# Kernel optimization log

Hardware: AMD Instinct MI355X
Metric: run time of the kernel (lower is better)

The kernel has to match this reference:

```python
import jax, jax.numpy as jnp
import numpy as np


def setup_inputs() -> dict:
    key = jax.random.key(0)
    k1, k2 = jax.random.split(key)
    b, n, d = 8, 4096, 128
    qk = jax.random.normal(k1, (b, n, d), dtype=jnp.float32)
    v = jax.random.normal(k2, (b, n, d), dtype=jnp.float32)
    return {"qk": qk, "v": v}


def reference(qk, v):
    # qk: [b, n, d] shared query/key tensor; v: [b, n, d]
    b, n, d = qk.shape
    # keys = L2-normalized qk (F.normalize eps=1e-12); queries = raw qk
    k = qk / jnp.maximum(jnp.linalg.norm(qk, axis=-1, keepdims=True), 1e-12)
    scores = jnp.einsum('bie,bje->bij', qk, k) * (d ** -0.5)  # [b, n, n]
    # mask self-attention on the diagonal with -inf
    eye = jnp.eye(n, dtype=bool)
    scores = jnp.where(eye[None, :, :], -jnp.inf, scores)
    attn = jax.nn.softmax(scores, axis=-1)
    out = jnp.einsum('bij,bje->bie', attn, v)  # [b, n, d]
    return out
```

## Files before the change

### kernel.cpp

```cpp
#include <hip/hip_runtime.h>
#include <hip/hip_bf16.h>
#include <stdint.h>

#define BATCH 8
#define SEQN  4096
#define DIM   128
#define NT    32

typedef __attribute__((ext_vector_type(16))) float f32x16;
typedef __bf16 bf16x8 __attribute__((ext_vector_type(8)));

#define GAS __attribute__((address_space(1)))
#define LAS __attribute__((address_space(3)))

__device__ __forceinline__ ushort f2b(float x) {
  union { float f; uint32_t u; } a; a.f = x;
  uint32_t r = a.u + 0x7fffu + ((a.u >> 16) & 1u);
  return (ushort)(r >> 16);
}
__device__ __forceinline__ uint32_t pkbf(float a, float b) {
  union { __bf16 h[2]; uint32_t u; } x;
  x.h[0] = (__bf16)a; x.h[1] = (__bf16)b;
  return x.u;
}


__global__ __launch_bounds__(256) void prep_qk(
    const float* __restrict__ qk, ushort* __restrict__ qfb, ushort* __restrict__ kfb) {
  __shared__ ushort qt_l[32 * 136];
  __shared__ ushort kt_l[32 * 136];
  const int g = blockIdx.x;
  const int t = threadIdx.x;
  const int r = t >> 3, s = t & 7;
  const float* src = qk + (size_t)g * 4096 + r * 128 + s * 16;
  float x[16];
  #pragma unroll
  for (int i = 0; i < 4; ++i) {
    float4 f = ((const float4*)src)[i];
    x[4*i] = f.x; x[4*i+1] = f.y; x[4*i+2] = f.z; x[4*i+3] = f.w;
  }
  float ss = 0.f;
  #pragma unroll
  for (int i = 0; i < 16; ++i) ss += x[i] * x[i];
  ss += __shfl_xor(ss, 1, 64);
  ss += __shfl_xor(ss, 2, 64);
  ss += __shfl_xor(ss, 4, 64);
  float rn = 1.0f / fmaxf(sqrtf(ss), 1e-12f);
  const float SC = 1.44269504088896340736f / 11.313708498984761f;
  float rs = rn * SC;
  #pragma unroll
  for (int j = 0; j < 16; ++j) {
    qt_l[r * 136 + s * 16 + j] = f2b(x[j]);
    kt_l[r * 136 + s * 16 + j] = f2b(x[j] * rs);
  }
  __syncthreads();
  #pragma unroll
  for (int p = 0; p < 2; ++p) {
    int sl = t + 256 * p;
    int qli = sl & 31, grp = sl >> 5;
    union { ushort u[8]; int4 v; } tq, tk;
    #pragma unroll
    for (int j = 0; j < 8; ++j) {
      tq.u[j] = qt_l[qli * 136 + grp * 8 + j];
      tk.u[j] = kt_l[qli * 136 + grp * 8 + j];
    }
    *(int4*)(qfb + (size_t)g * 4096 + sl * 8) = tq.v;
    *(int4*)(kfb + (size_t)g * 4096 + sl * 8) = tk.v;
  }
}

__global__ __launch_bounds__(256) void prep_v(
    const float* __restrict__ v, ushort* __restrict__ vfb) {
  __shared__ ushort vt_l[32 * 136];
  const int g = blockIdx.x;
  const int t = threadIdx.x;
  const int r = t >> 3, s = t & 7;
  const float* src = v + (size_t)g * 4096 + r * 128 + s * 16;
  #pragma unroll
  for (int i = 0; i < 4; ++i) {
    float4 f = ((const float4*)src)[i];
    vt_l[r * 136 + s * 16 + 4*i]     = f2b(f.x);
    vt_l[r * 136 + s * 16 + 4*i + 1] = f2b(f.y);
    vt_l[r * 136 + s * 16 + 4*i + 2] = f2b(f.z);
    vt_l[r * 136 + s * 16 + 4*i + 3] = f2b(f.w);
  }
  __syncthreads();
  #pragma unroll
  for (int p = 0; p < 2; ++p) {
    int sl = t + 256 * p;
    int qli = sl & 31, grp = sl >> 5;
    int db = grp >> 2, ks = (grp >> 1) & 1, hh = grp & 1;
    union { ushort u[8]; int4 v; } tv;
    #pragma unroll
    for (int j = 0; j < 8; ++j)
      tv.u[j] = vt_l[(16 * ks + 8 * hh + j) * 136 + 32 * db + qli];
    *(int4*)(vfb + (size_t)g * 4096 + sl * 8) = tv.v;
  }
}

__global__ __launch_bounds__(256, 2) void attn_kernel(
    const ushort* __restrict__ qfb, const ushort* __restrict__ kfb,
    const ushort* __restrict__ vfb, float* __restrict__ out) {
  __shared__ ushort lds[40960];

  const int tid = threadIdx.x;
  const int w  = tid >> 6;
  const int l  = tid & 63;
  const int ql = l & 31;
  const int hi = l >> 5;

  const int bidx  = blockIdx.x;
  const int batch = bidx & 7;
  const int qt    = bidx >> 3;
  const int q0    = qt * 64;
  const size_t cb = (size_t)batch * 128;

  const ushort* kq = kfb + (cb + w * 32) * 4096;
  const ushort* vq = vfb + (cb + w * 32) * 4096;
  ushort* myv = lds + w * 8192;
  ushort* ldsq = lds + 32768;

  {
    const ushort* qsrc = qfb + (cb + qt * 2) * 4096 + tid * 8;
    #pragma unroll
    for (int i = 0; i < 4; ++i)
      __builtin_amdgcn_global_load_lds((const GAS uint32_t*)(qsrc + i * 2048),
          (LAS uint32_t*)(ldsq + i * 2048 + tid * 8), 16, 0, 0);
  }

#define STAGE(bsel, t_) do {                                                   \
    const ushort* vsrc_ = vq + (size_t)(t_) * 4096 + l * 8;                    \
    ushort* vdst_ = myv + (bsel) * 4096 + l * 8;                               \
    _Pragma("unroll")                                                          \
    for (int i_ = 0; i_ < 8; ++i_)                                             \
      __builtin_amdgcn_global_load_lds((const GAS uint32_t*)(vsrc_ + i_ * 512),\
          (LAS uint32_t*)(vdst_ + i_ * 512), 16, 0, 0);                        \
  } while (0)

  STAGE(0, 0);
  bf16x8 kf[8];
  {
    const ushort* kt_p = kq + l * 8;
    #pragma unroll
    for (int kc = 0; kc < 8; ++kc) kf[kc] = *(const bf16x8*)(kt_p + kc * 512);
  }
  __syncthreads();

  f32x16 o[8];
  #pragma unroll
  for (int i = 0; i < 8; ++i)
    #pragma unroll
    for (int r = 0; r < 16; ++r) o[i][r] = 0.f;
  float lsum0 = 0.f, lsum1 = 0.f;

  int buf = 0;
  for (int t = 0; t < NT; ++t) {
    if (t + 1 < NT) STAGE(buf ^ 1, t + 1);

    bf16x8 pa[2][2];
    {
      f32x16 st;
      #pragma unroll
      for (int r = 0; r < 16; ++r) st[r] = 0.f;
      const ushort* qlp = ldsq + l * 8;
      __builtin_amdgcn_s_setprio(1);
      #pragma unroll
      for (int kc = 0; kc < 8; ++kc) {
        bf16x8 qf = *(const bf16x8*)(qlp + kc * 512);
        st = __builtin_amdgcn_mfma_f32_32x32x16_bf16(kf[kc], qf, st, 0, 0, 0);
      }
      __builtin_amdgcn_s_setprio(0);
      if (w * 1024 + t * 32 == q0) {
        #pragma unroll
        for (int r = 0; r < 16; ++r) {
          int crow = (r & 3) + 8 * (r >> 2) + 4 * hi;
          if (crow == ql) st[r] = -1e30f;
        }
      }
      float p[16]; float rs_ = 0.f;
      #pragma unroll
      for (int r = 0; r < 16; ++r) { p[r] = exp2f(st[r]); rs_ += p[r]; }
      lsum0 += rs_;
      uint32_t ww[4][2];
      #pragma unroll
      for (int g4 = 0; g4 < 4; ++g4) {
        ww[g4][0] = pkbf(p[4 * g4 + 0], p[4 * g4 + 1]);
        ww[g4][1] = pkbf(p[4 * g4 + 2], p[4 * g4 + 3]);
      }
      #pragma unroll
      for (int ks = 0; ks < 2; ++ks) {
        uint32_t a0 = ww[2 * ks][0], b0 = ww[2 * ks + 1][0];
        uint32_t a1 = ww[2 * ks][1], b1 = ww[2 * ks + 1][1];
        asm volatile("v_permlane32_swap_b32 %0, %1" : "+v"(a0), "+v"(b0));
        asm volatile("v_permlane32_swap_b32 %0, %1" : "+v"(a1), "+v"(b1));
        union { uint32_t u[4]; bf16x8 v; } pb;
        pb.u[0] = a0; pb.u[1] = a1; pb.u[2] = b0; pb.u[3] = b1;
        pa[0][ks] = pb.v;
      }
    }
    {
      f32x16 st;
      #pragma unroll
      for (int r = 0; r < 16; ++r) st[r] = 0.f;
      const ushort* qlp = ldsq + 4096 + l * 8;
      __builtin_amdgcn_s_setprio(1);
      #pragma unroll
      for (int kc = 0; kc < 8; ++kc) {
        bf16x8 qf = *(const bf16x8*)(qlp + kc * 512);
        st = __builtin_amdgcn_mfma_f32_32x32x16_bf16(kf[kc], qf, st, 0, 0, 0);
      }
      __builtin_amdgcn_s_setprio(0);
      if (t + 1 < NT) {
        const ushort* kt_p = kq + (size_t)(t + 1) * 4096 + l * 8;
        #pragma unroll
        for (int kc = 0; kc < 8; ++kc) kf[kc] = *(const bf16x8*)(kt_p + kc * 512);
      }
      if (w * 1024 + t * 32 == q0 + 32) {
        #pragma unroll
        for (int r = 0; r < 16; ++r) {
          int crow = (r & 3) + 8 * (r >> 2) + 4 * hi;
          if (crow == ql) st[r] = -1e30f;
        }
      }
      float p[16]; float rs_ = 0.f;
      #pragma unroll
      for (int r = 0; r < 16; ++r) { p[r] = exp2f(st[r]); rs_ += p[r]; }
      lsum1 += rs_;
      uint32_t ww[4][2];
      #pragma unroll
      for (int g4 = 0; g4 < 4; ++g4) {
        ww[g4][0] = pkbf(p[4 * g4 + 0], p[4 * g4 + 1]);
        ww[g4][1] = pkbf(p[4 * g4 + 2], p[4 * g4 + 3]);
      }
      #pragma unroll
      for (int ks = 0; ks < 2; ++ks) {
        uint32_t a0 = ww[2 * ks][0], b0 = ww[2 * ks + 1][0];
        uint32_t a1 = ww[2 * ks][1], b1 = ww[2 * ks + 1][1];
        asm volatile("v_permlane32_swap_b32 %0, %1" : "+v"(a0), "+v"(b0));
        asm volatile("v_permlane32_swap_b32 %0, %1" : "+v"(a1), "+v"(b1));
        union { uint32_t u[4]; bf16x8 v; } pb;
        pb.u[0] = a0; pb.u[1] = a1; pb.u[2] = b0; pb.u[3] = b1;
        pa[1][ks] = pb.v;
      }
    }

    asm volatile("s_waitcnt vmcnt(16)" ::: "memory");
    __builtin_amdgcn_sched_barrier(0);

    const ushort* vlp = myv + buf * 4096 + l * 8;
    __builtin_amdgcn_s_setprio(1);
    #pragma unroll
    for (int db = 0; db < 4; ++db)
      #pragma unroll
      for (int ks = 0; ks < 2; ++ks) {
        bf16x8 vv = *(const bf16x8*)(vlp + (db * 4 + ks * 2) * 256);
        o[db]     = __builtin_amdgcn_mfma_f32_32x32x16_bf16(vv, pa[0][ks], o[db],     0, 0, 0);
        o[4 + db] = __builtin_amdgcn_mfma_f32_32x32x16_bf16(vv, pa[1][ks], o[4 + db], 0, 0, 0);
      }
    __builtin_amdgcn_s_setprio(0);
    buf ^= 1;
  }
#undef STAGE

  __syncthreads();
  float* A  = (float*)lds;
  float* Bb = A + 8448;
  float* lt = A + 16896;
  float* Lf = A + 17408;

  lt[((w * 2 + hi) * 2 + 0) * 32 + ql] = lsum0;
  lt[((w * 2 + hi) * 2 + 1) * 32 + ql] = lsum1;
  __syncthreads();
  float L0 = 0.f, L1 = 0.f;
  #pragma unroll
  for (int i = 0; i < 8; ++i) {
    L0 += lt[(i * 2 + 0) * 32 + ql];
    L1 += lt[(i * 2 + 1) * 32 + ql];
  }
  if (w == 0 && hi == 0) { Lf[ql] = 1.0f / L0; Lf[32 + ql] = 1.0f / L1; }

  if (w == 3 || w == 1) {
    float* D = (w == 3) ? A : Bb;
    #pragma unroll
    for (int c = 0; c < 2; ++c)
      #pragma unroll
      for (int db = 0; db < 4; ++db)
        #pragma unroll
        for (int g4 = 0; g4 < 4; ++g4)
          *(float4*)(D + (32 * c + ql) * 132 + 32 * db + 8 * g4 + 4 * hi) =
              make_float4(o[c * 4 + db][4 * g4], o[c * 4 + db][4 * g4 + 1],
                          o[c * 4 + db][4 * g4 + 2], o[c * 4 + db][4 * g4 + 3]);
  }
  __syncthreads();
  if (w == 2 || w == 0) {
    float* D = (w == 2) ? A : Bb;
    #pragma unroll
    for (int c = 0; c < 2; ++c)
      #pragma unroll
      for (int db = 0; db < 4; ++db)
        #pragma unroll
        for (int g4 = 0; g4 < 4; ++g4) {
          float* ptr = D + (32 * c + ql) * 132 + 32 * db + 8 * g4 + 4 * hi;
          float4 tv = *(float4*)ptr;
          tv.x += o[c * 4 + db][4 * g4];
          tv.y += o[c * 4 + db][4 * g4 + 1];
          tv.z += o[c * 4 + db][4 * g4 + 2];
          tv.w += o[c * 4 + db][4 * g4 + 3];
          *(float4*)ptr = tv;
        }
  }
  __syncthreads();
  if (w == 0 || w == 2) {
    const int ch = w >> 1;
    float* outb = out + ((size_t)batch * SEQN + q0) * DIM;
    #pragma unroll
    for (int s2 = 0; s2 < 32; ++s2) {
      const int q = 32 * ch + s2;
      const float iv = Lf[q];
      float2 a2 = *(const float2*)(A + q * 132 + 2 * l);
      float2 b2 = *(const float2*)(Bb + q * 132 + 2 * l);
      *(float2*)(outb + (size_t)q * DIM + 2 * l) =
          make_float2((a2.x + b2.x) * iv, (a2.y + b2.y) * iv);
    }
  }
}

extern "C" void kernel_launch(void* const* d_in, const int* in_sizes, int n_in,
                              void* d_out, int out_size, void* d_ws, size_t ws_size,
                              hipStream_t stream) {
  (void)in_sizes; (void)n_in; (void)out_size; (void)ws_size;
  const float* qk = (const float*)d_in[0];
  const float* v  = (const float*)d_in[1];
  float* out = (float*)d_out;
  size_t nelem = (size_t)BATCH * SEQN * DIM;
  ushort* qfb = (ushort*)d_ws;
  ushort* kfb = qfb + nelem;
  ushort* vfb = kfb + nelem;
  prep_qk<<<BATCH * SEQN / 32, 256, 0, stream>>>(qk, qfb, kfb);
  prep_v <<<BATCH * SEQN / 32, 256, 0, stream>>>(v, vfb);
  attn_kernel<<<BATCH * (SEQN / 64), 256, 0, stream>>>(qfb, kfb, vfb, out);
}
```

Measured before the change: 115.1 us.

## Fuse prep kernels and interleave the two QK MFMA chains with the K prefetch

Merges the separate qk and v preprocessing kernels into a single launch. In the attention loop, the two 32-row score tiles are now computed with interleaved MFMA chains, and the next-tile K fragment loads are issued inside that loop instead of after it. Also switches to the raw exp2 intrinsic and uses a tree reduction for the row sums. The aim is to cut launch overhead, expose more independent MFMA work, and hide K load latency, at the cost of higher register pressure from two live accumulators plus the in-flight K loads.

Measured after the change: 99.04 us. -13.9%, faster.

```diff
diff --git a/kernel.cpp b/kernel.cpp
--- a/kernel.cpp
+++ b/kernel.cpp
@@ -25,75 +25,66 @@
 }
 
 
-__global__ __launch_bounds__(256) void prep_qk(
-    const float* __restrict__ qk, ushort* __restrict__ qfb, ushort* __restrict__ kfb) {
+__global__ __launch_bounds__(256) void prep_fused(
+    const float* __restrict__ qk, const float* __restrict__ v,
+    ushort* __restrict__ qfb, ushort* __restrict__ kfb, ushort* __restrict__ vfb) {
   __shared__ ushort qt_l[32 * 136];
   __shared__ ushort kt_l[32 * 136];
+  __shared__ ushort vt_l[32 * 136];
   const int g = blockIdx.x;
   const int t = threadIdx.x;
   const int r = t >> 3, s = t & 7;
-  const float* src = qk + (size_t)g * 4096 + r * 128 + s * 16;
-  float x[16];
-  #pragma unroll
-  for (int i = 0; i < 4; ++i) {
-    float4 f = ((const float4*)src)[i];
-    x[4*i] = f.x; x[4*i+1] = f.y; x[4*i+2] = f.z; x[4*i+3] = f.w;
-  }
-  float ss = 0.f;
-  #pragma unroll
-  for (int i = 0; i < 16; ++i) ss += x[i] * x[i];
-  ss += __shfl_xor(ss, 1, 64);
-  ss += __shfl_xor(ss, 2, 64);
-  ss += __shfl_xor(ss, 4, 64);
-  float rn = 1.0f / fmaxf(sqrtf(ss), 1e-12f);
-  const float SC = 1.44269504088896340736f / 11.313708498984761f;
-  float rs = rn * SC;
-  #pragma unroll
-  for (int j = 0; j < 16; ++j) {
-    qt_l[r * 136 + s * 16 + j] = f2b(x[j]);
-    kt_l[r * 136 + s * 16 + j] = f2b(x[j] * rs);
+  {
+    const float* src = qk + (size_t)g * 4096 + r * 128 + s * 16;
+    float x[16];
+    #pragma unroll
+    for (int i = 0; i < 4; ++i) {
+      float4 f = ((const float4*)src)[i];
+      x[4*i] = f.x; x[4*i+1] = f.y; x[4*i+2] = f.z; x[4*i+3] = f.w;
+    }
+    float ss = 0.f;
+    #pragma unroll
+    for (int i = 0; i < 16; ++i) ss += x[i] * x[i];
+    ss += __shfl_xor(ss, 1, 64);
+    ss += __shfl_xor(ss, 2, 64);
+    ss += __shfl_xor(ss, 4, 64);
+    float rn = 1.0f / fmaxf(sqrtf(ss), 1e-12f);
+    const float SC = 1.44269504088896340736f / 11.313708498984761f;
+    float rs = rn * SC;
+    #pragma unroll
+    for (int j = 0; j < 16; ++j) {
+      qt_l[r * 136 + s * 16 + j] = f2b(x[j]);
+      kt_l[r * 136 + s * 16 + j] = f2b(x[j] * rs);
+    }
+  }
+  {
+    const float* src = v + (size_t)g * 4096 + r * 128 + s * 16;
+    #pragma unroll
+    for (int i = 0; i < 4; ++i) {
+      float4 f = ((const float4*)src)[i];
+      vt_l[r * 136 + s * 16 + 4*i]     = f2b(f.x);
+      vt_l[r * 136 + s * 16 + 4*i + 1] = f2b(f.y);
+      vt_l[r * 136 + s * 16 + 4*i + 2] = f2b(f.z);
+      vt_l[r * 136 + s * 16 + 4*i + 3] = f2b(f.w);
+    }
   }
   __syncthreads();
   #pragma unroll
   for (int p = 0; p < 2; ++p) {
     int sl = t + 256 * p;
     int qli = sl & 31, grp = sl >> 5;
-    union { ushort u[8]; int4 v; } tq, tk;
+    union { ushort u[8]; int4 v; } tq, tk, tv;
     #pragma unroll
     for (int j = 0; j < 8; ++j) {
       tq.u[j] = qt_l[qli * 136 + grp * 8 + j];
       tk.u[j] = kt_l[qli * 136 + grp * 8 + j];
     }
+    int db = grp >> 2, ks = (grp >> 1) & 1, hh = grp & 1;
+    #pragma unroll
+    for (int j = 0; j < 8; ++j)
+      tv.u[j] = vt_l[(16 * ks + 8 * hh + j) * 136 + 32 * db + qli];
     *(int4*)(qfb + (size_t)g * 4096 + sl * 8) = tq.v;
     *(int4*)(kfb + (size_t)g * 4096 + sl * 8) = tk.v;
-  }
-}
-
-__global__ __launch_bounds__(256) void prep_v(
-    const float* __restrict__ v, ushort* __restrict__ vfb) {
-  __shared__ ushort vt_l[32 * 136];
-  const int g = blockIdx.x;
-  const int t = threadIdx.x;
-  const int r = t >> 3, s = t & 7;
-  const float* src = v + (size_t)g * 4096 + r * 128 + s * 16;
-  #pragma unroll
-  for (int i = 0; i < 4; ++i) {
-    float4 f = ((const float4*)src)[i];
-    vt_l[r * 136 + s * 16 + 4*i]     = f2b(f.x);
-    vt_l[r * 136 + s * 16 + 4*i + 1] = f2b(f.y);
-    vt_l[r * 136 + s * 16 + 4*i + 2] = f2b(f.z);
-    vt_l[r * 136 + s * 16 + 4*i + 3] = f2b(f.w);
-  }
-  __syncthreads();
-  #pragma unroll
-  for (int p = 0; p < 2; ++p) {
-    int sl = t + 256 * p;
-    int qli = sl & 31, grp = sl >> 5;
-    int db = grp >> 2, ks = (grp >> 1) & 1, hh = grp & 1;
-    union { ushort u[8]; int4 v; } tv;
-    #pragma unroll
-    for (int j = 0; j < 8; ++j)
-      tv.u[j] = vt_l[(16 * ks + 8 * hh + j) * 136 + 32 * db + qli];
     *(int4*)(vfb + (size_t)g * 4096 + sl * 8) = tv.v;
   }
 }
@@ -151,97 +142,89 @@
   for (int i = 0; i < 8; ++i)
     #pragma unroll
     for (int r = 0; r < 16; ++r) o[i][r] = 0.f;
-  float lsum0 = 0.f, lsum1 = 0.f;
+  float ls0 = 0.f, ls1 = 0.f;
 
   int buf = 0;
   for (int t = 0; t < NT; ++t) {
     if (t + 1 < NT) STAGE(buf ^ 1, t + 1);
-
-    bf16x8 pa[2][2];
+    const bool pfK = (t + 1 < NT);
+    const ushort* kp_n = kq + (size_t)(t + 1) * 4096 + l * 8;
+
+    f32x16 st0, st1;
+    #pragma unroll
+    for (int r = 0; r < 16; ++r) { st0[r] = 0.f; st1[r] = 0.f; }
+    const ushort* qlp = ldsq + l * 8;
+    __builtin_amdgcn_s_setprio(1);
+    #pragma unroll
+    for (int kc = 0; kc < 8; ++kc) {
+      bf16x8 q0f = *(const bf16x8*)(qlp + kc * 512);
+      bf16x8 q1f = *(const bf16x8*)(qlp + 4096 + kc * 512);
+      st0 = __builtin_amdgcn_mfma_f32_32x32x16_bf16(kf[kc], q0f, st0, 0, 0, 0);
+      st1 = __builtin_amdgcn_mfma_f32_32x32x16_bf16(kf[kc], q1f, st1, 0, 0, 0);
+      if (pfK) kf[kc] = *(const bf16x8*)(kp_n + kc * 512);
+    }
+    __builtin_amdgcn_s_setprio(0);
+
+    const int kvb = w * 1024 + t * 32;
+    if (kvb == q0) {
+      #pragma unroll
+      for (int r = 0; r < 16; ++r) {
+        int crow = (r & 3) + 8 * (r >> 2) + 4 * hi;
+        if (crow == ql) st0[r] = -1e30f;
+      }
+    }
+    if (kvb == q0 + 32) {
+      #pragma unroll
+      for (int r = 0; r < 16; ++r) {
+        int crow = (r & 3) + 8 * (r >> 2) + 4 * hi;
+        if (crow == ql) st1[r] = -1e30f;
+      }
+    }
+
+    float p0[16], p1[16];
+    #pragma unroll
+    for (int r = 0; r < 16; ++r) {
+      p0[r] = __builtin_amdgcn_exp2f(st0[r]);
+      p1[r] = __builtin_amdgcn_exp2f(st1[r]);
+    }
     {
-      f32x16 st;
-      #pragma unroll
-      for (int r = 0; r < 16; ++r) st[r] = 0.f;
-      const ushort* qlp = ldsq + l * 8;
-      __builtin_amdgcn_s_setprio(1);
-      #pragma unroll
-      for (int kc = 0; kc < 8; ++kc) {
-        bf16x8 qf = *(const bf16x8*)(qlp + kc * 512);
-        st = __builtin_amdgcn_mfma_f32_32x32x16_bf16(kf[kc], qf, st, 0, 0, 0);
-      }
-      __builtin_amdgcn_s_setprio(0);
-      if (w * 1024 + t * 32 == q0) {
-        #pragma unroll
-        for (int r = 0; r < 16; ++r) {
-          int crow = (r & 3) + 8 * (r >> 2) + 4 * hi;
-          if (crow == ql) st[r] = -1e30f;
-        }
-      }
-      float p[16]; float rs_ = 0.f;
-      #pragma unroll
-      for (int r = 0; r < 16; ++r) { p[r] = exp2f(st[r]); rs_ += p[r]; }
-      lsum0 += rs_;
-      uint32_t ww[4][2];
-      #pragma unroll
-      for (int g4 = 0; g4 < 4; ++g4) {
-        ww[g4][0] = pkbf(p[4 * g4 + 0], p[4 * g4 + 1]);
-        ww[g4][1] = pkbf(p[4 * g4 + 2], p[4 * g4 + 3]);
-      }
-      #pragma unroll
-      for (int ks = 0; ks < 2; ++ks) {
-        uint32_t a0 = ww[2 * ks][0], b0 = ww[2 * ks + 1][0];
-        uint32_t a1 = ww[2 * ks][1], b1 = ww[2 * ks + 1][1];
-        asm volatile("v_permlane32_swap_b32 %0, %1" : "+v"(a0), "+v"(b0));
-        asm volatile("v_permlane32_swap_b32 %0, %1" : "+v"(a1), "+v"(b1));
-        union { uint32_t u[4]; bf16x8 v; } pb;
-        pb.u[0] = a0; pb.u[1] = a1; pb.u[2] = b0; pb.u[3] = b1;
-        pa[0][ks] = pb.v;
-      }
-    }
-    {
-      f32x16 st;
-      #pragma unroll
-      for (int r = 0; r < 16; ++r) st[r] = 0.f;
-      const ushort* qlp = ldsq + 4096 + l * 8;
-      __builtin_amdgcn_s_setprio(1);
-      #pragma unroll
-      for (int kc = 0; kc < 8; ++kc) {
-        bf16x8 qf = *(const bf16x8*)(qlp + kc * 512);
-        st = __builtin_amdgcn_mfma_f32_32x32x16_bf16(kf[kc], qf, st, 0, 0, 0);
-      }
-      __builtin_amdgcn_s_setprio(0);
-      if (t + 1 < NT) {
-        const ushort* kt_p = kq + (size_t)(t + 1) * 4096 + l * 8;
-        #pragma unroll
-        for (int kc = 0; kc < 8; ++kc) kf[kc] = *(const bf16x8*)(kt_p + kc * 512);
-      }
-      if (w * 1024 + t * 32 == q0 + 32) {
-        #pragma unroll
-        for (int r = 0; r < 16; ++r) {
-          int crow = (r & 3) + 8 * (r >> 2) + 4 * hi;
-          if (crow == ql) st[r] = -1e30f;
-        }
-      }
-      float p[16]; float rs_ = 0.f;
-      #pragma unroll
-      for (int r = 0; r < 16; ++r) { p[r] = exp2f(st[r]); rs_ += p[r]; }
-      lsum1 += rs_;
-      uint32_t ww[4][2];
-      #pragma unroll
-      for (int g4 = 0; g4 < 4; ++g4) {
-        ww[g4][0] = pkbf(p[4 * g4 + 0], p[4 * g4 + 1]);
-        ww[g4][1] = pkbf(p[4 * g4 + 2], p[4 * g4 + 3]);
-      }
-      #pragma unroll
-      for (int ks = 0; ks < 2; ++ks) {
-        uint32_t a0 = ww[2 * ks][0], b0 = ww[2 * ks + 1][0];
-        uint32_t a1 = ww[2 * ks][1], b1 = ww[2 * ks + 1][1];
-        asm volatile("v_permlane32_swap_b32 %0, %1" : "+v"(a0), "+v"(b0));
-        asm volatile("v_permlane32_swap_b32 %0, %1" : "+v"(a1), "+v"(b1));
-        union { uint32_t u[4]; bf16x8 v; } pb;
-        pb.u[0] = a0; pb.u[1] = a1; pb.u[2] = b0; pb.u[3] = b1;
-        pa[1][ks] = pb.v;
-      }
+      float a = (p0[0] + p0[1]) + (p0[2] + p0[3]);
+      float b = (p0[4] + p0[5]) + (p0[6] + p0[7]);
+      float c = (p0[8] + p0[9]) + (p0[10] + p0[11]);
+      float d = (p0[12] + p0[13]) + (p0[14] + p0[15]);
+      ls0 += (a + b) + (c + d);
+      float e = (p1[0] + p1[1]) + (p1[2] + p1[3]);
+      float f = (p1[4] + p1[5]) + (p1[6] + p1[7]);
+      float g = (p1[8] + p1[9]) + (p1[10] + p1[11]);
+      float h = (p1[12] + p1[13]) + (p1[14] + p1[15]);
+      ls1 += (e + f) + (g + h);
+    }
+
+    uint32_t w0[4][2], w1[4][2];
+    #pragma unroll
+    for (int g4 = 0; g4 < 4; ++g4) {
+      w0[g4][0] = pkbf(p0[4 * g4 + 0], p0[4 * g4 + 1]);
+      w0[g4][1] = pkbf(p0[4 * g4 + 2], p0[4 * g4 + 3]);
+      w1[g4][0] = pkbf(p1[4 * g4 + 0], p1[4 * g4 + 1]);
+      w1[g4][1] = pkbf(p1[4 * g4 + 2], p1[4 * g4 + 3]);
+    }
+    bf16x8 pa0[2], pa1[2];
+    #pragma unroll
+    for (int ks = 0; ks < 2; ++ks) {
+      uint32_t a0 = w0[2 * ks][0], b0 = w0[2 * ks + 1][0];
+      uint32_t a1 = w0[2 * ks][1], b1 = w0[2 * ks + 1][1];
+      asm volatile("v_permlane32_swap_b32 %0, %1" : "+v"(a0), "+v"(b0));
+      asm volatile("v_permlane32_swap_b32 %0, %1" : "+v"(a1), "+v"(b1));
+      union { uint32_t u[4]; bf16x8 v; } pb;
+      pb.u[0] = a0; pb.u[1] = a1; pb.u[2] = b0; pb.u[3] = b1;
+      pa0[ks] = pb.v;
+      uint32_t c0 = w1[2 * ks][0], d0 = w1[2 * ks + 1][0];
+      uint32_t c1 = w1[2 * ks][1], d1 = w1[2 * ks + 1][1];
+      asm volatile("v_permlane32_swap_b32 %0, %1" : "+v"(c0), "+v"(d0));
+      asm volatile("v_permlane32_swap_b32 %0, %1" : "+v"(c1), "+v"(d1));
+      union { uint32_t u[4]; bf16x8 v; } pc;
+      pc.u[0] = c0; pc.u[1] = c1; pc.u[2] = d0; pc.u[3] = d1;
+      pa1[ks] = pc.v;
     }
 
     asm volatile("s_waitcnt vmcnt(16)" ::: "memory");
@@ -254,8 +237,8 @@
       #pragma unroll
       for (int ks = 0; ks < 2; ++ks) {
         bf16x8 vv = *(const bf16x8*)(vlp + (db * 4 + ks * 2) * 256);
-        o[db]     = __builtin_amdgcn_mfma_f32_32x32x16_bf16(vv, pa[0][ks], o[db],     0, 0, 0);
-        o[4 + db] = __builtin_amdgcn_mfma_f32_32x32x16_bf16(vv, pa[1][ks], o[4 + db], 0, 0, 0);
+        o[db]     = __builtin_amdgcn_mfma_f32_32x32x16_bf16(vv, pa0[ks], o[db],     0, 0, 0);
+        o[4 + db] = __builtin_amdgcn_mfma_f32_32x32x16_bf16(vv, pa1[ks], o[4 + db], 0, 0, 0);
       }
     __builtin_amdgcn_s_setprio(0);
     buf ^= 1;
@@ -268,8 +251,8 @@
   float* lt = A + 16896;
   float* Lf = A + 17408;
 
-  lt[((w * 2 + hi) * 2 + 0) * 32 + ql] = lsum0;
-  lt[((w * 2 + hi) * 2 + 1) * 32 + ql] = lsum1;
+  lt[((w * 2 + hi) * 2 + 0) * 32 + ql] = ls0;
+  lt[((w * 2 + hi) * 2 + 1) * 32 + ql] = ls1;
   __syncthreads();
   float L0 = 0.f, L1 = 0.f;
   #pragma unroll
@@ -336,7 +319,6 @@
   ushort* qfb = (ushort*)d_ws;
   ushort* kfb = qfb + nelem;
   ushort* vfb = kfb + nelem;
-  prep_qk<<<BATCH * SEQN / 32, 256, 0, stream>>>(qk, qfb, kfb);
-  prep_v <<<BATCH * SEQN / 32, 256, 0, stream>>>(v, vfb);
+  prep_fused<<<BATCH * SEQN / 32, 256, 0, stream>>>(qk, v, qfb, kfb, vfb);
   attn_kernel<<<BATCH * (SEQN / 64), 256, 0, stream>>>(qfb, kfb, vfb, out);
 }
```
